# Kernel optimization log

Hardware: AMD Instinct MI355X
Metric: run time of the kernel (lower is better)

The kernel has to match this reference:

```python
import jax, jax.numpy as jnp
import numpy as np

IN_FEATURES = 512
OUT_FEATURES = 256
BATCH = 1024


def setup_inputs() -> dict:
    key = jax.random.key(0)
    k1, k2, k3, k4 = jax.random.split(key, 4)
    n_lower = IN_FEATURES * (IN_FEATURES - 1) // 2  # strictly-lower triangle count
    return {
        "inputs": jax.random.normal(k1, (BATCH, IN_FEATURES), dtype=jnp.float32),
        "weight": jax.random.normal(k2, (OUT_FEATURES, 1, IN_FEATURES), dtype=jnp.float32),
        "L_diags": jax.random.uniform(k3, (OUT_FEATURES, IN_FEATURES), dtype=jnp.float32),
        "L_lower": jax.random.normal(k4, (OUT_FEATURES, n_lower), dtype=jnp.float32) * 0.05,
    }


def _build_L(L_diags, L_lower):
    # Per-class lower-triangular matrix: diag = L_diags**2, strict lower = L_lower.
    K, d = L_diags.shape
    ri, ci = np.tril_indices(d, k=-1)  # static index pattern (row-major, matches torch.tril_indices)
    diag_idx = jnp.arange(d)
    L = jnp.zeros((K, d, d), dtype=L_diags.dtype)
    L = L.at[:, diag_idx, diag_idx].set(jnp.square(L_diags))
    L = L.at[:, ri, ci].set(L_lower)
    return L  # [K, d, d]


def reference(inputs, weight, L_diags, L_lower):
    L = _build_L(L_diags, L_lower)                      # [K, d, d]
    pinputs = jnp.einsum('bd,kde->kbe', inputs, L)      # [K, B, d]
    pweights = jnp.einsum('kod,kde->koe', weight, L)    # [K, 1, d]
    dist = pinputs - pweights                           # broadcast over B -> [K, B, d]
    out = jnp.sqrt(jnp.sum(jnp.square(dist), axis=2))   # torch.norm(dim=2) -> [K, B]
    return out.T                                        # [B, K]
```

## Files before the change

### kernel.cpp

```cpp
#include <hip/hip_runtime.h>
#include <hip/hip_bf16.h>
#include <math.h>

#define B_SZ   1024
#define D_SZ   512
#define KC_SZ  256
#define NLOW   130816

#define STEP_ELEMS  8192
#define NSTEPS      20
#define CLASS_ELEMS (NSTEPS * STEP_ELEMS)

#define OFF_XP     (size_t)(KC_SZ * CLASS_ELEMS * 2)
#define OFF_TPART  (OFF_XP + 64 * STEP_ELEMS * 2)
#define OFF_T      (OFF_TPART + (size_t)KC_SZ * 8 * 512 * 4)
#define WS_NEED    (OFF_T + (size_t)KC_SZ * 512 * 4)

typedef __attribute__((ext_vector_type(4))) float  f32x4;
typedef __attribute__((ext_vector_type(8))) __bf16 bf16x8;

__global__ __launch_bounds__(256)
void prep_x(const float* __restrict__ X, __hip_bfloat16* __restrict__ Xp) {
    const int pg  = blockIdx.x;
    const int mt  = pg >> 3, kch = pg & 7;
    __bf16* out = (__bf16*)Xp + (size_t)pg * STEP_ELEMS;
    const int tid = threadIdx.x;
    #pragma unroll
    for (int i = 0; i < 4; ++i) {
        const int line = tid + i * 256;
        const int wmg = line >> 9, mi = (line >> 7) & 3, h = (line >> 6) & 1;
        const int lane = line & 63, q = lane >> 4, c = lane & 15;
        const int row = mt * 128 + wmg * 64 + mi * 16 + c;
        const float* src = X + (size_t)row * D_SZ + kch * 64 + h * 32 + q * 8;
        f32x4 v0 = ((const f32x4*)src)[0];
        f32x4 v1 = ((const f32x4*)src)[1];
        bf16x8 p;
        #pragma unroll
        for (int j = 0; j < 4; ++j) { p[j] = (__bf16)v0[j]; p[j + 4] = (__bf16)v1[j]; }
        *(bf16x8*)(out + line * 8) = p;
    }
}

__device__ __forceinline__ int sbase_of(int ct) { return ct * (9 - ct); }

__global__ __launch_bounds__(256)
void prep_b(const float* __restrict__ Ldiag,
            const float* __restrict__ Llow,
            const float* __restrict__ W,
            __hip_bfloat16* __restrict__ Bp,
            float* __restrict__ tpart) {
    __shared__ float Ls[64][65];
    __shared__ float Wsm[64];
    __shared__ float pt[4][64];

    const int bid = blockIdx.x;
    const int kc  = bid >> 6;
    const int et  = (bid >> 3) & 7;
    const int dt  = bid & 7;
    const int ct  = et >> 1;
    const int dmin = ct << 1;
    if (dt < dmin) return;

    const int s  = sbase_of(ct) + (dt - dmin);
    const int e0 = et << 6, d0 = dt << 6;
    const int tid = threadIdx.x;

    __bf16* page = (__bf16*)Bp + (size_t)kc * CLASS_ELEMS + (size_t)s * STEP_ELEMS;
    float*  tp   = tpart + ((size_t)(kc * 8 + dt)) * 512;

    const int qp = tid >> 5;
    const int ep = tid & 31;
    const int el0 = ((et & 1) << 6) + (ep << 1);
    const int h = qp >> 2, q = qp & 3;
    const int line0 = ((((el0 >> 6) * 4 + ((el0 >> 4) & 3)) * 2 + h) * 64) + q * 16 + (el0 & 15);
    __bf16* dst = page + line0 * 8;

    if (d0 + 64 <= e0) {
        bf16x8 z;
        #pragma unroll
        for (int i = 0; i < 8; ++i) z[i] = (__bf16)0.f;
        *(bf16x8*)dst = z;
        *(bf16x8*)(dst + 8) = z;
        if (tid < 64) tp[et * 64 + tid] = 0.f;
        return;
    }

    if (tid < 64) Wsm[tid] = W[(size_t)kc * D_SZ + d0 + tid];

    const int r  = tid >> 2;
    const int cq = (tid & 3) << 4;
    const float* lowb = Llow + (size_t)kc * NLOW;
    const int d   = d0 + r;
    const int tri = (d * (d - 1)) >> 1;

    if (d0 >= e0 + 64) {
        #pragma unroll
        for (int j = 0; j < 16; ++j) Ls[r][cq + j] = lowb[tri + e0 + cq + j];
    } else {
        const float* diagb = Ldiag + (size_t)kc * D_SZ;
        #pragma unroll
        for (int j = 0; j < 16; ++j) {
            const int e = e0 + cq + j;
            float v = 0.f;
            if (e < d)       v = lowb[tri + e];
            else if (e == d) { float qd = diagb[d]; v = qd * qd; }
            Ls[r][cq + j] = v;
        }
    }
    __syncthreads();

    bf16x8 p0, p1;
    #pragma unroll
    for (int j = 0; j < 8; ++j) {
        p0[j] = (__bf16)Ls[qp * 8 + j][ep * 2];
        p1[j] = (__bf16)Ls[qp * 8 + j][ep * 2 + 1];
    }
    *(bf16x8*)dst = p0;
    *(bf16x8*)(dst + 8) = p1;

    {
        const int part = tid >> 6, ei = tid & 63;
        float sum = 0.f;
        #pragma unroll
        for (int j = 0; j < 16; ++j)
            sum += Wsm[part * 16 + j] * Ls[part * 16 + j][ei];
        pt[part][ei] = sum;
    }
    __syncthreads();
    if (tid < 64)
        tp[et * 64 + tid] = pt[0][tid] + pt[1][tid] + pt[2][tid] + pt[3][tid];
}

__global__ __launch_bounds__(256)
void t_reduce(const float* __restrict__ tpart, float* __restrict__ Tv) {
    const int idx = blockIdx.x * 256 + threadIdx.x;
    const int kc = idx >> 9, e = idx & 511;
    const int ct = e >> 7;
    float s = 0.f;
    for (int dt = ct << 1; dt < 8; ++dt)
        s += tpart[((size_t)(kc * 8 + dt)) * 512 + e];
    Tv[idx] = s;
}

__device__ __forceinline__ int kch_of(int s) {
    return (s < 8) ? s : (s < 14) ? s - 6 : (s < 18) ? s - 10 : s - 12;
}

__global__ __launch_bounds__(256, 2)
void gml2_main(const __hip_bfloat16* __restrict__ Xp,
               const __hip_bfloat16* __restrict__ Bp,
               const float* __restrict__ Tv,
               float* __restrict__ Out) {
    __shared__ float osum[2][128];

    const int tid = threadIdx.x;
    const int bx  = blockIdx.x;
    const int xcd = bx & 7;
    const int g   = bx >> 3;
    const int kc  = xcd * 32 + (g >> 3);
    const int mt  = g & 7;

    const int lane = tid & 63;
    const int wave = tid >> 6;
    const int wmg  = wave & 1;
    const int wng  = wave >> 1;
    const int c    = lane & 15;
    const int q    = lane >> 4;

    const __bf16* pA = (const __bf16*)Xp + (size_t)(mt * 8) * STEP_ELEMS;
    const __bf16* pB = (const __bf16*)Bp + (size_t)kc * CLASS_ELEMS;

    int aoff[4][2], boff[4][2];
    #pragma unroll
    for (int mi = 0; mi < 4; ++mi)
        #pragma unroll
        for (int h = 0; h < 2; ++h)
            aoff[mi][h] = ((((wmg * 4 + mi) * 2 + h) * 64) + lane) * 8;
    #pragma unroll
    for (int ni = 0; ni < 4; ++ni)
        #pragma unroll
        for (int h = 0; h < 2; ++h)
            boff[ni][h] = ((((wng * 4 + ni) * 2 + h) * 64) + lane) * 8;

    f32x4 acc[4][4];
    #pragma unroll
    for (int mi = 0; mi < 4; ++mi)
        #pragma unroll
        for (int ni = 0; ni < 4; ++ni)
            acc[mi][ni] = (f32x4){0.f, 0.f, 0.f, 0.f};
    float rsum[16];
    #pragma unroll
    for (int i = 0; i < 16; ++i) rsum[i] = 0.f;

    bf16x8 fa0[4][2], fb0[4][2], fa1[4][2], fb1[4][2];

#define LOAD_A(FA, KCH) { const __bf16* p_ = pA + (KCH) * STEP_ELEMS;          \
    _Pragma("unroll") for (int mi = 0; mi < 4; ++mi)                           \
    _Pragma("unroll") for (int h = 0; h < 2; ++h)                              \
        FA[mi][h] = *(const bf16x8*)(p_ + aoff[mi][h]); }
#define LOAD_B(FB, SP) { const __bf16* p_ = pB + (SP) * STEP_ELEMS;            \
    _Pragma("unroll") for (int ni = 0; ni < 4; ++ni)                           \
    _Pragma("unroll") for (int h = 0; h < 2; ++h)                              \
        FB[ni][h] = *(const bf16x8*)(p_ + boff[ni][h]); }
#define MFMA_STEP(FA, FB)                                                      \
    _Pragma("unroll") for (int mi = 0; mi < 4; ++mi)                           \
    _Pragma("unroll") for (int ni = 0; ni < 4; ++ni)                           \
    _Pragma("unroll") for (int h = 0; h < 2; ++h)                              \
        acc[mi][ni] = __builtin_amdgcn_mfma_f32_16x16x32_bf16(                 \
            FA[mi][h], FB[ni][h], acc[mi][ni], 0, 0, 0);

#define FOLD(CT) {                                                             \
    float tv_[4];                                                              \
    _Pragma("unroll") for (int ni = 0; ni < 4; ++ni)                           \
        tv_[ni] = Tv[kc * 512 + (CT) * 128 + wng * 64 + ni * 16 + c];          \
    _Pragma("unroll") for (int mi = 0; mi < 4; ++mi)                           \
    _Pragma("unroll") for (int ni = 0; ni < 4; ++ni)                           \
    _Pragma("unroll") for (int r = 0; r < 4; ++r) {                            \
        float y_ = acc[mi][ni][r] - tv_[ni];                                   \
        rsum[mi * 4 + r] += y_ * y_;                                           \
        acc[mi][ni][r] = 0.f; } }

    LOAD_A(fa0, 0); LOAD_B(fb0, 0);

    for (int s = 0; s < NSTEPS; s += 2) {
        if (s == 8)       { FOLD(0); }
        else if (s == 14) { FOLD(1); }
        else if (s == 18) { FOLD(2); }

        LOAD_A(fa1, kch_of(s + 1)); LOAD_B(fb1, s + 1);
        MFMA_STEP(fa0, fb0);
        if (s + 2 < NSTEPS) { LOAD_A(fa0, kch_of(s + 2)); LOAD_B(fb0, s + 2); }
        MFMA_STEP(fa1, fb1);
    }
    FOLD(3);

    #pragma unroll
    for (int i = 0; i < 16; ++i) {
        float v = rsum[i];
        v += __shfl_xor(v, 1, 64);
        v += __shfl_xor(v, 2, 64);
        v += __shfl_xor(v, 4, 64);
        v += __shfl_xor(v, 8, 64);
        rsum[i] = v;
    }
    if (c == 0) {
        #pragma unroll
        for (int mi = 0; mi < 4; ++mi)
            #pragma unroll
            for (int r = 0; r < 4; ++r)
                osum[wng][wmg * 64 + mi * 16 + q * 4 + r] = rsum[mi * 4 + r];
    }
    __syncthreads();
    if (tid < 128) {
        float v = osum[0][tid] + osum[1][tid];
        Out[(size_t)(mt * 128 + tid) * KC_SZ + kc] = sqrtf(v);
    }
}

#define FLDA 40
#define BM 128
#define BN 128
__device__ __forceinline__ void fstep_map(int s, int& ct, int& k0) {
    if (s < 16)      { ct = 0; k0 = s * 32; }
    else if (s < 28) { ct = 1; k0 = 128 + (s - 16) * 32; }
    else if (s < 36) { ct = 2; k0 = 256 + (s - 28) * 32; }
    else             { ct = 3; k0 = 384 + (s - 36) * 32; }
}
__global__ __launch_bounds__(256, 2)
void gml2_fallback(const float* __restrict__ X, const float* __restrict__ W,
                   const float* __restrict__ Ldiag, const float* __restrict__ Llow,
                   float* __restrict__ Out) {
    __shared__ __bf16 As[BM * FLDA];
    __shared__ __bf16 Bs[BN * FLDA];
    __shared__ float  Ws[D_SZ];
    __shared__ float  osum[2][BM];
    const int tid = threadIdx.x;
    const int bx  = blockIdx.x;
    const int xcd = bx & 7;
    const int g   = bx >> 3;
    const int kc  = xcd * 32 + (g >> 3);
    const int mt  = g & 7;
    const int lane = tid & 63, wave = tid >> 6;
    const int wm = (wave & 1) * 64, wn = (wave >> 1) * 64;
    const int c = lane & 15, q = lane >> 4;
    const int am = tid >> 1, akh = (tid & 1) << 4;
    const float* xrow = X + (size_t)(mt * BM + am) * D_SZ;
    const float* wrow = W + (size_t)kc * D_SZ;
    const int be = tid & 127, bd = (tid >> 7) << 4;
    const float* lowbase  = Llow  + (size_t)kc * NLOW;
    const float* diagbase = Ldiag + (size_t)kc * D_SZ;
    if (tid < 128) ((f32x4*)Ws)[tid] = ((const f32x4*)wrow)[tid];
    float rsum[16];
    #pragma unroll
    for (int i = 0; i < 16; ++i) rsum[i] = 0.f;
    f32x4 acc[4][4];
    #pragma unroll
    for (int mi = 0; mi < 4; ++mi)
        #pragma unroll
        for (int ni = 0; ni < 4; ++ni) acc[mi][ni] = (f32x4){0.f, 0.f, 0.f, 0.f};
    f32x4 xr[4];
    float bb[16];
    auto prefetch = [&](int s) {
        int pct, pk0; fstep_map(s, pct, pk0);
        const int pe0 = pct * BN;
        const float* xp = xrow + pk0 + akh;
        #pragma unroll
        for (int i = 0; i < 4; ++i) xr[i] = ((const f32x4*)xp)[i];
        const int e = pe0 + be, d0 = pk0 + bd;
        int tri = (d0 * (d0 - 1)) >> 1;
        if (pk0 >= pe0 + BN) {
            #pragma unroll
            for (int j = 0; j < 16; ++j) { bb[j] = lowbase[tri + e]; tri += d0 + j; }
        } else {
            #pragma unroll
            for (int j = 0; j < 16; ++j) {
                const int d = d0 + j;
                float val = 0.f;
                if (d > e)       val = lowbase[tri + e];
                else if (d == e) { float dq = diagbase[d]; val = dq * dq; }
                bb[j] = val; tri += d;
            }
        }
    };
    prefetch(0);
    __syncthreads();
    int cur_ct = 0;
    for (int s = 0; s < 40; ++s) {
        int ct, k0; fstep_map(s, ct, k0);
        if (ct != cur_ct) {
            #pragma unroll
            for (int mi = 0; mi < 4; ++mi)
                #pragma unroll
                for (int ni = 0; ni < 4; ++ni)
                    #pragma unroll
                    for (int r = 0; r < 4; ++r) {
                        float y = acc[mi][ni][r];
                        rsum[mi * 4 + r] += y * y;
                        acc[mi][ni][r] = 0.f;
                    }
            cur_ct = ct;
        }
        bf16x8 ap0, ap1;
        {
            const f32x4* wsp = (const f32x4*)&Ws[k0 + akh];
            #pragma unroll
            for (int i = 0; i < 4; ++i) {
                f32x4 wv = wsp[i];
                #pragma unroll
                for (int l = 0; l < 4; ++l) {
                    float v = xr[i][l] - wv[l];
                    int idx = i * 4 + l;
                    if (idx < 8) ap0[idx] = (__bf16)v;
                    else         ap1[idx - 8] = (__bf16)v;
                }
            }
        }
        bf16x8 bp0, bp1;
        #pragma unroll
        for (int j = 0; j < 8; ++j) { bp0[j] = (__bf16)bb[j]; bp1[j] = (__bf16)bb[j + 8]; }
        __syncthreads();
        *(bf16x8*)&As[am * FLDA + akh]     = ap0;
        *(bf16x8*)&As[am * FLDA + akh + 8] = ap1;
        *(bf16x8*)&Bs[be * FLDA + bd]      = bp0;
        *(bf16x8*)&Bs[be * FLDA + bd + 8]  = bp1;
        if (s + 1 < 40) prefetch(s + 1);
        __syncthreads();
        bf16x8 af[4], bfr[4];
        #pragma unroll
        for (int mi = 0; mi < 4; ++mi)
            af[mi] = *(const bf16x8*)&As[(wm + mi * 16 + c) * FLDA + q * 8];
        #pragma unroll
        for (int ni = 0; ni < 4; ++ni)
            bfr[ni] = *(const bf16x8*)&Bs[(wn + ni * 16 + c) * FLDA + q * 8];
        #pragma unroll
        for (int mi = 0; mi < 4; ++mi)
            #pragma unroll
            for (int ni = 0; ni < 4; ++ni)
                acc[mi][ni] = __builtin_amdgcn_mfma_f32_16x16x32_bf16(
                    af[mi], bfr[ni], acc[mi][ni], 0, 0, 0);
    }
    #pragma unroll
    for (int mi = 0; mi < 4; ++mi)
        #pragma unroll
        for (int ni = 0; ni < 4; ++ni)
            #pragma unroll
            for (int r = 0; r < 4; ++r) {
                float y = acc[mi][ni][r];
                rsum[mi * 4 + r] += y * y;
            }
    #pragma unroll
    for (int i = 0; i < 16; ++i) {
        float s = rsum[i];
        s += __shfl_xor(s, 1, 64);
        s += __shfl_xor(s, 2, 64);
        s += __shfl_xor(s, 4, 64);
        s += __shfl_xor(s, 8, 64);
        rsum[i] = s;
    }
    const int wnIdx = wave >> 1;
    if (c == 0) {
        #pragma unroll
        for (int mi = 0; mi < 4; ++mi)
            #pragma unroll
            for (int r = 0; r < 4; ++r)
                osum[wnIdx][wm + mi * 16 + q * 4 + r] = rsum[mi * 4 + r];
    }
    __syncthreads();
    if (tid < BM) {
        float s = osum[0][tid] + osum[1][tid];
        Out[(size_t)(mt * BM + tid) * KC_SZ + kc] = sqrtf(s);
    }
}

extern "C" void kernel_launch(void* const* d_in, const int* in_sizes, int n_in,
                              void* d_out, int out_size, void* d_ws, size_t ws_size,
                              hipStream_t stream) {
    const float* X  = (const float*)d_in[0];
    const float* W  = (const float*)d_in[1];
    const float* Ld = (const float*)d_in[2];
    const float* Ll = (const float*)d_in[3];
    float* Out = (float*)d_out;

    if (ws_size >= WS_NEED) {
        __hip_bfloat16* Bp    = (__hip_bfloat16*)d_ws;
        __hip_bfloat16* Xp    = (__hip_bfloat16*)((char*)d_ws + OFF_XP);
        float*          tpart = (float*)((char*)d_ws + OFF_TPART);
        float*          Tvv   = (float*)((char*)d_ws + OFF_T);
        prep_x  <<<dim3(64),            dim3(256), 0, stream>>>(X, Xp);
        prep_b  <<<dim3(KC_SZ * 64),    dim3(256), 0, stream>>>(Ld, Ll, W, Bp, tpart);
        t_reduce<<<dim3(512),           dim3(256), 0, stream>>>(tpart, Tvv);
        gml2_main<<<dim3(KC_SZ * 8),    dim3(256), 0, stream>>>(Xp, Bp, Tvv, Out);
    } else {
        gml2_fallback<<<dim3(KC_SZ * 8), dim3(256), 0, stream>>>(X, W, Ld, Ll, Out);
    }
}
```

Before: 357.3 us.

## Fuse T reduction into main kernel, restructure prep_b loop and deepen MFMA prefetch

Drops the t_reduce launch and has the main GEMM kernel sum the per-d-tile partial W·L terms itself at each fold. prep_b now runs one block per (class, d-tile) and loops over e-tiles, with a register prefetch of the next tile's gather, instead of launching one block per tile with early exits. prep_x uses one line per thread across more blocks. The main loop now processes two k-steps per phase with a 4-deep register fragment buffer. The trade-offs are fewer launches and less idle-block overhead against more register pressure and redundant partial-sum reads in every main block.

```diff
diff --git a/kernel.cpp b/kernel.cpp
--- a/kernel.cpp
+++ b/kernel.cpp
@@ -13,35 +13,29 @@
 
 #define OFF_XP     (size_t)(KC_SZ * CLASS_ELEMS * 2)
 #define OFF_TPART  (OFF_XP + 64 * STEP_ELEMS * 2)
-#define OFF_T      (OFF_TPART + (size_t)KC_SZ * 8 * 512 * 4)
-#define WS_NEED    (OFF_T + (size_t)KC_SZ * 512 * 4)
+#define WS_NEED    (OFF_TPART + (size_t)KC_SZ * 8 * 512 * 4)
 
 typedef __attribute__((ext_vector_type(4))) float  f32x4;
 typedef __attribute__((ext_vector_type(8))) __bf16 bf16x8;
 
+__device__ __forceinline__ int sbase_of(int ct) { return ct * (9 - ct); }
+
 __global__ __launch_bounds__(256)
 void prep_x(const float* __restrict__ X, __hip_bfloat16* __restrict__ Xp) {
-    const int pg  = blockIdx.x;
-    const int mt  = pg >> 3, kch = pg & 7;
-    __bf16* out = (__bf16*)Xp + (size_t)pg * STEP_ELEMS;
-    const int tid = threadIdx.x;
-    #pragma unroll
-    for (int i = 0; i < 4; ++i) {
-        const int line = tid + i * 256;
-        const int wmg = line >> 9, mi = (line >> 7) & 3, h = (line >> 6) & 1;
-        const int lane = line & 63, q = lane >> 4, c = lane & 15;
-        const int row = mt * 128 + wmg * 64 + mi * 16 + c;
-        const float* src = X + (size_t)row * D_SZ + kch * 64 + h * 32 + q * 8;
-        f32x4 v0 = ((const f32x4*)src)[0];
-        f32x4 v1 = ((const f32x4*)src)[1];
-        bf16x8 p;
-        #pragma unroll
-        for (int j = 0; j < 4; ++j) { p[j] = (__bf16)v0[j]; p[j + 4] = (__bf16)v1[j]; }
-        *(bf16x8*)(out + line * 8) = p;
-    }
-}
-
-__device__ __forceinline__ int sbase_of(int ct) { return ct * (9 - ct); }
+    const int line = blockIdx.x * 256 + threadIdx.x;
+    const int pg = line >> 10, ll = line & 1023;
+    const int mt = pg >> 3, kch = pg & 7;
+    const int wmg = ll >> 9, mi = (ll >> 7) & 3, h = (ll >> 6) & 1;
+    const int lane = ll & 63, q = lane >> 4, c = lane & 15;
+    const int row = mt * 128 + wmg * 64 + mi * 16 + c;
+    const float* src = X + (size_t)row * D_SZ + kch * 64 + h * 32 + q * 8;
+    f32x4 v0 = ((const f32x4*)src)[0];
+    f32x4 v1 = ((const f32x4*)src)[1];
+    bf16x8 p;
+    #pragma unroll
+    for (int j = 0; j < 4; ++j) { p[j] = (__bf16)v0[j]; p[j + 4] = (__bf16)v1[j]; }
+    *(bf16x8*)((__bf16*)Xp + (size_t)line * 8) = p;
+}
 
 __global__ __launch_bounds__(256)
 void prep_b(const float* __restrict__ Ldiag,
@@ -54,102 +48,107 @@
     __shared__ float pt[4][64];
 
     const int bid = blockIdx.x;
-    const int kc  = bid >> 6;
-    const int et  = (bid >> 3) & 7;
+    const int kc  = bid >> 3;
     const int dt  = bid & 7;
-    const int ct  = et >> 1;
-    const int dmin = ct << 1;
-    if (dt < dmin) return;
-
-    const int s  = sbase_of(ct) + (dt - dmin);
-    const int e0 = et << 6, d0 = dt << 6;
+    const int d0  = dt << 6;
+    const int etmax = dt | 1;
     const int tid = threadIdx.x;
 
-    __bf16* page = (__bf16*)Bp + (size_t)kc * CLASS_ELEMS + (size_t)s * STEP_ELEMS;
-    float*  tp   = tpart + ((size_t)(kc * 8 + dt)) * 512;
-
+    if (tid < 64) Wsm[tid] = W[(size_t)kc * D_SZ + d0 + tid];
+
+    const float* lowb  = Llow  + (size_t)kc * NLOW;
+    const float* diagb = Ldiag + (size_t)kc * D_SZ;
+    float* tp = tpart + ((size_t)(kc * 8 + dt)) * 512;
+    __bf16* cls = (__bf16*)Bp + (size_t)kc * CLASS_ELEMS;
+
+    const int r  = tid >> 2;
+    const int cq = (tid & 3) << 4;
+    const int d  = d0 + r;
+    const int tri = (d * (d - 1)) >> 1;
     const int qp = tid >> 5;
     const int ep = tid & 31;
-    const int el0 = ((et & 1) << 6) + (ep << 1);
-    const int h = qp >> 2, q = qp & 3;
-    const int line0 = ((((el0 >> 6) * 4 + ((el0 >> 4) & 3)) * 2 + h) * 64) + q * 16 + (el0 & 15);
-    __bf16* dst = page + line0 * 8;
-
-    if (d0 + 64 <= e0) {
-        bf16x8 z;
-        #pragma unroll
-        for (int i = 0; i < 8; ++i) z[i] = (__bf16)0.f;
-        *(bf16x8*)dst = z;
-        *(bf16x8*)(dst + 8) = z;
-        if (tid < 64) tp[et * 64 + tid] = 0.f;
-        return;
-    }
-
-    if (tid < 64) Wsm[tid] = W[(size_t)kc * D_SZ + d0 + tid];
-
-    const int r  = tid >> 2;
-    const int cq = (tid & 3) << 4;
-    const float* lowb = Llow + (size_t)kc * NLOW;
-    const int d   = d0 + r;
-    const int tri = (d * (d - 1)) >> 1;
-
-    if (d0 >= e0 + 64) {
-        #pragma unroll
-        for (int j = 0; j < 16; ++j) Ls[r][cq + j] = lowb[tri + e0 + cq + j];
-    } else {
-        const float* diagb = Ldiag + (size_t)kc * D_SZ;
-        #pragma unroll
-        for (int j = 0; j < 16; ++j) {
-            const int e = e0 + cq + j;
-            float v = 0.f;
-            if (e < d)       v = lowb[tri + e];
-            else if (e == d) { float qd = diagb[d]; v = qd * qd; }
-            Ls[r][cq + j] = v;
-        }
-    }
-    __syncthreads();
-
-    bf16x8 p0, p1;
-    #pragma unroll
-    for (int j = 0; j < 8; ++j) {
-        p0[j] = (__bf16)Ls[qp * 8 + j][ep * 2];
-        p1[j] = (__bf16)Ls[qp * 8 + j][ep * 2 + 1];
-    }
-    *(bf16x8*)dst = p0;
-    *(bf16x8*)(dst + 8) = p1;
-
-    {
-        const int part = tid >> 6, ei = tid & 63;
-        float sum = 0.f;
-        #pragma unroll
-        for (int j = 0; j < 16; ++j)
-            sum += Wsm[part * 16 + j] * Ls[part * 16 + j][ei];
-        pt[part][ei] = sum;
-    }
-    __syncthreads();
-    if (tid < 64)
-        tp[et * 64 + tid] = pt[0][tid] + pt[1][tid] + pt[2][tid] + pt[3][tid];
-}
-
-__global__ __launch_bounds__(256)
-void t_reduce(const float* __restrict__ tpart, float* __restrict__ Tv) {
-    const int idx = blockIdx.x * 256 + threadIdx.x;
-    const int kc = idx >> 9, e = idx & 511;
-    const int ct = e >> 7;
-    float s = 0.f;
-    for (int dt = ct << 1; dt < 8; ++dt)
-        s += tpart[((size_t)(kc * 8 + dt)) * 512 + e];
-    Tv[idx] = s;
-}
-
-__device__ __forceinline__ int kch_of(int s) {
-    return (s < 8) ? s : (s < 14) ? s - 6 : (s < 18) ? s - 10 : s - 12;
-}
+    const int h  = qp >> 2, q = qp & 3;
+
+    auto gather = [&](int et, float* vv) {
+        const int e0 = et << 6;
+        if (et < dt) {
+            const float* base = lowb + tri + e0 + cq;
+            #pragma unroll
+            for (int j = 0; j < 16; ++j) vv[j] = base[j];
+        } else {
+            #pragma unroll
+            for (int j = 0; j < 16; ++j) {
+                const int e = e0 + cq + j;
+                float v = 0.f;
+                if (e < d)       v = lowb[tri + e];
+                else if (e == d) { float qd = diagb[d]; v = qd * qd; }
+                vv[j] = v;
+            }
+        }
+    };
+
+    float v0[16];
+    gather(0, v0);
+
+    for (int et = 0; et <= etmax; ++et) {
+        const bool zt = (et > dt);
+        if (!zt) {
+            #pragma unroll
+            for (int j = 0; j < 16; ++j) Ls[r][cq + j] = v0[j];
+        }
+        __syncthreads();
+
+        float v1[16];
+        const bool pf = (et + 1 <= etmax) && (et + 1 <= dt);
+        if (pf) gather(et + 1, v1);
+
+        const int ct = et >> 1;
+        const int sp = sbase_of(ct) + (dt - (ct << 1));
+        const int el0 = ((et & 1) << 6) + (ep << 1);
+        const int line0 = ((((el0 >> 6) * 4 + ((el0 >> 4) & 3)) * 2 + h) * 64)
+                          + q * 16 + (el0 & 15);
+        __bf16* dst = cls + (size_t)sp * STEP_ELEMS + line0 * 8;
+
+        if (zt) {
+            bf16x8 z;
+            #pragma unroll
+            for (int i = 0; i < 8; ++i) z[i] = (__bf16)0.f;
+            *(bf16x8*)dst = z;
+            *(bf16x8*)(dst + 8) = z;
+            __syncthreads();
+            if (tid < 64) tp[et * 64 + tid] = 0.f;
+        } else {
+            bf16x8 p0, p1;
+            #pragma unroll
+            for (int j = 0; j < 8; ++j) {
+                p0[j] = (__bf16)Ls[qp * 8 + j][ep * 2];
+                p1[j] = (__bf16)Ls[qp * 8 + j][ep * 2 + 1];
+            }
+            *(bf16x8*)dst = p0;
+            *(bf16x8*)(dst + 8) = p1;
+            {
+                const int part = tid >> 6, ei = tid & 63;
+                float sum = 0.f;
+                #pragma unroll
+                for (int j = 0; j < 16; ++j)
+                    sum += Wsm[part * 16 + j] * Ls[part * 16 + j][ei];
+                pt[part][ei] = sum;
+            }
+            __syncthreads();
+            if (tid < 64)
+                tp[et * 64 + tid] = pt[0][tid] + pt[1][tid] + pt[2][tid] + pt[3][tid];
+        }
+        #pragma unroll
+        for (int j = 0; j < 16; ++j) v0[j] = v1[j];
+    }
+}
+
+__constant__ __device__ const int PH_KCH[10] = {0,2,4,6, 2,4,6, 4,6, 6};
 
 __global__ __launch_bounds__(256, 2)
 void gml2_main(const __hip_bfloat16* __restrict__ Xp,
                const __hip_bfloat16* __restrict__ Bp,
-               const float* __restrict__ Tv,
+               const float* __restrict__ tpart,
                float* __restrict__ Out) {
     __shared__ float osum[2][128];
 
@@ -174,13 +173,13 @@
     #pragma unroll
     for (int mi = 0; mi < 4; ++mi)
         #pragma unroll
-        for (int h = 0; h < 2; ++h)
-            aoff[mi][h] = ((((wmg * 4 + mi) * 2 + h) * 64) + lane) * 8;
+        for (int hh = 0; hh < 2; ++hh)
+            aoff[mi][hh] = ((((wmg * 4 + mi) * 2 + hh) * 64) + lane) * 8;
     #pragma unroll
     for (int ni = 0; ni < 4; ++ni)
         #pragma unroll
-        for (int h = 0; h < 2; ++h)
-            boff[ni][h] = ((((wng * 4 + ni) * 2 + h) * 64) + lane) * 8;
+        for (int hh = 0; hh < 2; ++hh)
+            boff[ni][hh] = ((((wng * 4 + ni) * 2 + hh) * 64) + lane) * 8;
 
     f32x4 acc[4][4];
     #pragma unroll
@@ -192,47 +191,66 @@
     #pragma unroll
     for (int i = 0; i < 16; ++i) rsum[i] = 0.f;
 
-    bf16x8 fa0[4][2], fb0[4][2], fa1[4][2], fb1[4][2];
-
-#define LOAD_A(FA, KCH) { const __bf16* p_ = pA + (KCH) * STEP_ELEMS;          \
-    _Pragma("unroll") for (int mi = 0; mi < 4; ++mi)                           \
-    _Pragma("unroll") for (int h = 0; h < 2; ++h)                              \
-        FA[mi][h] = *(const bf16x8*)(p_ + aoff[mi][h]); }
-#define LOAD_B(FB, SP) { const __bf16* p_ = pB + (SP) * STEP_ELEMS;            \
-    _Pragma("unroll") for (int ni = 0; ni < 4; ++ni)                           \
-    _Pragma("unroll") for (int h = 0; h < 2; ++h)                              \
-        FB[ni][h] = *(const bf16x8*)(p_ + boff[ni][h]); }
-#define MFMA_STEP(FA, FB)                                                      \
-    _Pragma("unroll") for (int mi = 0; mi < 4; ++mi)                           \
-    _Pragma("unroll") for (int ni = 0; ni < 4; ++ni)                           \
-    _Pragma("unroll") for (int h = 0; h < 2; ++h)                              \
-        acc[mi][ni] = __builtin_amdgcn_mfma_f32_16x16x32_bf16(                 \
-            FA[mi][h], FB[ni][h], acc[mi][ni], 0, 0, 0);
-
-#define FOLD(CT) {                                                             \
-    float tv_[4];                                                              \
-    _Pragma("unroll") for (int ni = 0; ni < 4; ++ni)                           \
-        tv_[ni] = Tv[kc * 512 + (CT) * 128 + wng * 64 + ni * 16 + c];          \
-    _Pragma("unroll") for (int mi = 0; mi < 4; ++mi)                           \
-    _Pragma("unroll") for (int ni = 0; ni < 4; ++ni)                           \
-    _Pragma("unroll") for (int r = 0; r < 4; ++r) {                            \
-        float y_ = acc[mi][ni][r] - tv_[ni];                                   \
-        rsum[mi * 4 + r] += y_ * y_;                                           \
-        acc[mi][ni][r] = 0.f; } }
-
-    LOAD_A(fa0, 0); LOAD_B(fb0, 0);
-
-    for (int s = 0; s < NSTEPS; s += 2) {
-        if (s == 8)       { FOLD(0); }
-        else if (s == 14) { FOLD(1); }
-        else if (s == 18) { FOLD(2); }
-
-        LOAD_A(fa1, kch_of(s + 1)); LOAD_B(fb1, s + 1);
-        MFMA_STEP(fa0, fb0);
-        if (s + 2 < NSTEPS) { LOAD_A(fa0, kch_of(s + 2)); LOAD_B(fb0, s + 2); }
-        MFMA_STEP(fa1, fb1);
-    }
-    FOLD(3);
+    bf16x8 FA[4][4], FB[4][4];
+
+    auto fold = [&](int ct) {
+        float tv_[4];
+        #pragma unroll
+        for (int ni = 0; ni < 4; ++ni) {
+            const int e = ct * 128 + wng * 64 + ni * 16 + c;
+            float s_ = 0.f;
+            for (int dtv = ct << 1; dtv < 8; ++dtv)
+                s_ += tpart[((size_t)(kc * 8 + dtv)) * 512 + e];
+            tv_[ni] = s_;
+        }
+        #pragma unroll
+        for (int mi = 0; mi < 4; ++mi)
+            #pragma unroll
+            for (int ni = 0; ni < 4; ++ni)
+                #pragma unroll
+                for (int rr = 0; rr < 4; ++rr) {
+                    float y_ = acc[mi][ni][rr] - tv_[ni];
+                    rsum[mi * 4 + rr] += y_ * y_;
+                    acc[mi][ni][rr] = 0.f;
+                }
+    };
+
+    #pragma unroll
+    for (int kk = 0; kk < 4; ++kk) {
+        const __bf16* pa = pA + (0 + (kk >> 1)) * STEP_ELEMS;
+        const __bf16* pb = pB + (0 + (kk >> 1)) * STEP_ELEMS;
+        #pragma unroll
+        for (int mi = 0; mi < 4; ++mi) FA[mi][kk] = *(const bf16x8*)(pa + aoff[mi][kk & 1]);
+        #pragma unroll
+        for (int ni = 0; ni < 4; ++ni) FB[ni][kk] = *(const bf16x8*)(pb + boff[ni][kk & 1]);
+    }
+
+    #pragma unroll
+    for (int p = 0; p < 10; ++p) {
+        #pragma unroll
+        for (int kk = 0; kk < 4; ++kk) {
+            #pragma unroll
+            for (int mi = 0; mi < 4; ++mi)
+                #pragma unroll
+                for (int ni = 0; ni < 4; ++ni)
+                    acc[mi][ni] = __builtin_amdgcn_mfma_f32_16x16x32_bf16(
+                        FA[mi][kk], FB[ni][kk], acc[mi][ni], 0, 0, 0);
+            if (p + 1 < 10) {
+                const __bf16* pa = pA + (PH_KCH[p + 1] + (kk >> 1)) * STEP_ELEMS;
+                const __bf16* pb = pB + (2 * (p + 1) + (kk >> 1)) * STEP_ELEMS;
+                #pragma unroll
+                for (int mi = 0; mi < 4; ++mi)
+                    FA[mi][kk] = *(const bf16x8*)(pa + aoff[mi][kk & 1]);
+                #pragma unroll
+                for (int ni = 0; ni < 4; ++ni)
+                    FB[ni][kk] = *(const bf16x8*)(pb + boff[ni][kk & 1]);
+            }
+        }
+        if (p == 3)      fold(0);
+        else if (p == 6) fold(1);
+        else if (p == 8) fold(2);
+        else if (p == 9) fold(3);
+    }
 
     #pragma unroll
     for (int i = 0; i < 16; ++i) {
@@ -247,8 +265,8 @@
         #pragma unroll
         for (int mi = 0; mi < 4; ++mi)
             #pragma unroll
-            for (int r = 0; r < 4; ++r)
-                osum[wng][wmg * 64 + mi * 16 + q * 4 + r] = rsum[mi * 4 + r];
+            for (int rr = 0; rr < 4; ++rr)
+                osum[wng][wmg * 64 + mi * 16 + q * 4 + rr] = rsum[mi * 4 + rr];
     }
     __syncthreads();
     if (tid < 128) {
@@ -425,11 +443,9 @@
         __hip_bfloat16* Bp    = (__hip_bfloat16*)d_ws;
         __hip_bfloat16* Xp    = (__hip_bfloat16*)((char*)d_ws + OFF_XP);
         float*          tpart = (float*)((char*)d_ws + OFF_TPART);
-        float*          Tvv   = (float*)((char*)d_ws + OFF_T);
-        prep_x  <<<dim3(64),            dim3(256), 0, stream>>>(X, Xp);
-        prep_b  <<<dim3(KC_SZ * 64),    dim3(256), 0, stream>>>(Ld, Ll, W, Bp, tpart);
-        t_reduce<<<dim3(512),           dim3(256), 0, stream>>>(tpart, Tvv);
-        gml2_main<<<dim3(KC_SZ * 8),    dim3(256), 0, stream>>>(Xp, Bp, Tvv, Out);
+        prep_x  <<<dim3(256),         dim3(256), 0, stream>>>(X, Xp);
+        prep_b  <<<dim3(KC_SZ * 8),   dim3(256), 0, stream>>>(Ld, Ll, W, Bp, tpart);
+        gml2_main<<<dim3(KC_SZ * 8),  dim3(256), 0, stream>>>(Xp, Bp, tpart, Out);
     } else {
         gml2_fallback<<<dim3(KC_SZ * 8), dim3(256), 0, stream>>>(X, W, Ld, Ll, Out);
     }
```

Measured after the change: 577.3 us. 1.62x slower.
